# Kernel optimization log

Hardware: AMD Instinct MI355X
Metric: run time of the kernel (lower is better)

## Reference

```python
import jax, jax.numpy as jnp
import numpy as np

N_NODES = 100000
N_EDGES = 1000000
D_IN = 64
D_OUT = 64


def setup_inputs() -> dict:
    key = jax.random.key(0)
    k_x, k_e, k_w, k_b = jax.random.split(key, 4)
    x = jax.random.normal(k_x, (N_NODES, D_IN), dtype=jnp.float32)
    edge_index = jax.random.randint(k_e, (2, N_EDGES), 0, N_NODES, dtype=jnp.int64)
    # degrees of destination nodes (what the caller is expected to supply);
    # clamp to >=1 to avoid division by zero for isolated nodes
    deg = jax.ops.segment_sum(jnp.ones((N_EDGES,), jnp.float32), edge_index[1], num_segments=N_NODES)
    node_degrees = jnp.maximum(deg, 1.0)
    W = jax.random.normal(k_w, (D_OUT, D_IN), dtype=jnp.float32) * (1.0 / np.sqrt(D_IN))
    b = jax.random.normal(k_b, (D_OUT,), dtype=jnp.float32) * 0.01
    return {"x": x, "edge_index": edge_index, "node_degrees": node_degrees, "W": W, "b": b}


def reference(x, edge_index, node_degrees, W, b):
    # Original does argsort+cumsum+boundary segment-sum; mathematically this is
    # a scatter-add of gathered neighbor features into dst, i.e. a segment sum.
    src, dst = edge_index[0], edge_index[1]
    agg = jax.ops.segment_sum(x[src], dst, num_segments=x.shape[0])  # [N, D_IN]
    mean = agg / node_degrees[:, None]
    return mean @ W.T + b  # [N, D_OUT]
```

## Files before the change

### kernel.cpp

```cpp
#include <hip/hip_runtime.h>


#define D 64
#define BSHIFT 6
#define BNODES (1 << BSHIFT)
#define CAP 1024
#define GTHREADS 512
#define PERTHREAD (CAP / GTHREADS)
#define PXW_THREADS 512
#define MAXB 2048

__device__ inline int detect_stride_block(const unsigned* __restrict__ words,
                                          int E, int* sflag) {
    int t = threadIdx.x;
    if (t < 64) {
        unsigned v = (t < E) ? words[2 * t + 1] : 0u;
        int any = __any(v != 0u);
        if (t == 0) *sflag = any ? 1 : 2;
    }
    __syncthreads();
    return *sflag;
}

__device__ inline unsigned pack_bf16(float a, float b) {
    unsigned ua = __float_as_uint(a), ub = __float_as_uint(b);
    ua += 0x7fffu + ((ua >> 16) & 1u);
    ub += 0x7fffu + ((ub >> 16) & 1u);
    return (ua >> 16) | (ub & 0xffff0000u);
}

__global__ __launch_bounds__(PXW_THREADS, 4) void partition_xw_kernel(
        const unsigned* __restrict__ ewords, int* __restrict__ cursor,
        unsigned* __restrict__ pairs, uint2* __restrict__ spill,
        int* __restrict__ spillCnt,
        const float* __restrict__ x, const float* __restrict__ W,
        unsigned* __restrict__ y2, int E, int N, int nb, int pblocks) {
    __shared__ __align__(16) char smem[52240];
    int t = threadIdx.x;

    if ((int)blockIdx.x < pblocks) {
        int* lhist = (int*)smem;
        int* lbase = lhist + MAXB;
        int* sflag = lbase + MAXB;
        int s = detect_stride_block(ewords, E, sflag);
        int base = blockIdx.x * 8192;
        for (int i = t; i < nb; i += PXW_THREADS) lhist[i] = 0;
        __syncthreads();
        unsigned pv[16]; int bk[16];
        #pragma unroll
        for (int k = 0; k < 16; ++k) {
            int e = base + k * PXW_THREADS + t;
            bk[k] = -1;
            if (e < E) {
                unsigned src = ewords[(size_t)e * s];
                unsigned dst = ewords[((size_t)E + e) * s];
                bk[k] = (int)(dst >> BSHIFT);
                pv[k] = src | ((dst & (BNODES - 1)) << 17);
                atomicAdd(&lhist[bk[k]], 1);
            }
        }
        __syncthreads();
        for (int hb = t; hb < nb; hb += PXW_THREADS) {
            int cc = lhist[hb];
            if (cc) lbase[hb] = atomicAdd(&cursor[hb], cc);
            lhist[hb] = 0;
        }
        __syncthreads();
        #pragma unroll
        for (int k = 0; k < 16; ++k) {
            if (bk[k] >= 0) {
                int lpos = lbase[bk[k]] + atomicAdd(&lhist[bk[k]], 1);
                if (lpos < CAP) {
                    pairs[(size_t)bk[k] * CAP + lpos] = pv[k];
                } else {
                    int si = atomicAdd(spillCnt, 1);
                    unsigned dst = ((unsigned)bk[k] << BSHIFT) | (pv[k] >> 17);
                    spill[si] = make_uint2(pv[k] & 0x1FFFFu, dst);
                }
            }
        }
    } else {
        float* Wt = (float*)smem;
        float* xs = Wt + 64 * 68;
        for (int i = t; i < 64 * 64; i += PXW_THREADS) {
            int o = i >> 6, k = i & 63;
            Wt[k * 68 + o] = W[i];
        }
        int base = ((int)blockIdx.x - pblocks) * 128;
        int row = t >> 4, c4 = (t & 15) * 4;
        #pragma unroll
        for (int r = 0; r < 4; ++r) {
            int nl = row + r * 32;
            int n = base + nl;
            float4 v = {0.f, 0.f, 0.f, 0.f};
            if (n < N) v = *(const float4*)(x + (size_t)n * 64 + c4);
            *(float4*)&xs[nl * 68 + c4] = v;
        }
        __syncthreads();
        int o4 = (t & 15) * 4, nl4 = (t >> 4) * 4;
        float acc[4][4];
        #pragma unroll
        for (int i = 0; i < 4; ++i)
            #pragma unroll
            for (int j = 0; j < 4; ++j) acc[i][j] = 0.f;
        #pragma unroll 2
        for (int k0 = 0; k0 < 64; k0 += 4) {
            float a[4][4], wv[4][4];
            #pragma unroll
            for (int i = 0; i < 4; ++i)
                *(float4*)a[i] = *(const float4*)&xs[(nl4 + i) * 68 + k0];
            #pragma unroll
            for (int dk = 0; dk < 4; ++dk)
                *(float4*)wv[dk] = *(const float4*)&Wt[(k0 + dk) * 68 + o4];
            #pragma unroll
            for (int i = 0; i < 4; ++i)
                #pragma unroll
                for (int j = 0; j < 4; ++j)
                    acc[i][j] += a[i][0] * wv[0][j] + a[i][1] * wv[1][j]
                               + a[i][2] * wv[2][j] + a[i][3] * wv[3][j];
        }
        int n0 = base + nl4;
        #pragma unroll
        for (int i = 0; i < 4; ++i) {
            if (n0 + i < N) {
                uint2 p;
                p.x = pack_bf16(acc[i][0], acc[i][1]);
                p.y = pack_bf16(acc[i][2], acc[i][3]);
                *(uint2*)(y2 + (size_t)(n0 + i) * 32 + (o4 >> 1)) = p;
            }
        }
    }
}

__global__ __launch_bounds__(GTHREADS) void bucket_gather(
        const unsigned* __restrict__ y2, const unsigned* __restrict__ pairs,
        const int* __restrict__ cursor, const uint2* __restrict__ spill,
        const int* __restrict__ spillCnt,
        const float* __restrict__ deg, const float* __restrict__ b,
        float* __restrict__ out, int N) {
    __shared__ unsigned list[CAP];
    __shared__ int cnt[BNODES], st[BNODES], sc[BNODES];
    int t = threadIdx.x;
    int bkt = blockIdx.x, base = bkt << BSHIFT;
    int total = cursor[bkt];
    int cn = total < CAP ? total : CAP;
    int node = t >> 3, c = t & 7;
    float4 bv0 = ((const float4*)b)[c * 2];
    float4 bv1 = ((const float4*)b)[c * 2 + 1];

    if (t < BNODES) cnt[t] = 0;
    __syncthreads();
    unsigned pv[PERTHREAD];
    #pragma unroll
    for (int j = 0; j < PERTHREAD; ++j) {
        int i = t + j * GTHREADS;
        pv[j] = (i < cn) ? pairs[(size_t)bkt * CAP + i] : 0xFFFFFFFFu;
        if (pv[j] != 0xFFFFFFFFu) atomicAdd(&cnt[pv[j] >> 17], 1);
    }
    __syncthreads();
    if (t < 64) {
        int v = cnt[t];
        #pragma unroll
        for (int off = 1; off < 64; off <<= 1) {
            int u = __shfl_up(v, off);
            if (t >= off) v += u;
        }
        st[t] = v - cnt[t]; sc[t] = v - cnt[t];
    }
    __syncthreads();
    #pragma unroll
    for (int j = 0; j < PERTHREAD; ++j) {
        if (pv[j] != 0xFFFFFFFFu) {
            int pos = atomicAdd(&sc[pv[j] >> 17], 1);
            list[pos] = pv[j] & 0x1FFFFu;
        }
    }
    __syncthreads();

    int scnt = *spillCnt;

    int n = base + node;
    int s0 = st[node], e1 = s0 + cnt[node];
    float a0 = 0.f, a1 = 0.f, a2 = 0.f, a3 = 0.f;
    float a4 = 0.f, a5 = 0.f, a6 = 0.f, a7 = 0.f;
    float b0 = 0.f, b1 = 0.f, b2 = 0.f, b3 = 0.f;
    float b4 = 0.f, b5 = 0.f, b6 = 0.f, b7 = 0.f;
    int i = s0;
    for (; i + 1 < e1; i += 2) {
        unsigned s0v = list[i], s1v = list[i + 1];
        uint4 u0 = *(const uint4*)(y2 + (size_t)s0v * 32 + c * 4);
        uint4 u1 = *(const uint4*)(y2 + (size_t)s1v * 32 + c * 4);
        a0 += __uint_as_float(u0.x << 16);
        a1 += __uint_as_float(u0.x & 0xffff0000u);
        a2 += __uint_as_float(u0.y << 16);
        a3 += __uint_as_float(u0.y & 0xffff0000u);
        a4 += __uint_as_float(u0.z << 16);
        a5 += __uint_as_float(u0.z & 0xffff0000u);
        a6 += __uint_as_float(u0.w << 16);
        a7 += __uint_as_float(u0.w & 0xffff0000u);
        b0 += __uint_as_float(u1.x << 16);
        b1 += __uint_as_float(u1.x & 0xffff0000u);
        b2 += __uint_as_float(u1.y << 16);
        b3 += __uint_as_float(u1.y & 0xffff0000u);
        b4 += __uint_as_float(u1.z << 16);
        b5 += __uint_as_float(u1.z & 0xffff0000u);
        b6 += __uint_as_float(u1.w << 16);
        b7 += __uint_as_float(u1.w & 0xffff0000u);
    }
    if (i < e1) {
        unsigned sv = list[i];
        uint4 u = *(const uint4*)(y2 + (size_t)sv * 32 + c * 4);
        a0 += __uint_as_float(u.x << 16);
        a1 += __uint_as_float(u.x & 0xffff0000u);
        a2 += __uint_as_float(u.y << 16);
        a3 += __uint_as_float(u.y & 0xffff0000u);
        a4 += __uint_as_float(u.z << 16);
        a5 += __uint_as_float(u.z & 0xffff0000u);
        a6 += __uint_as_float(u.w << 16);
        a7 += __uint_as_float(u.w & 0xffff0000u);
    }
    a0 += b0; a1 += b1; a2 += b2; a3 += b3;
    a4 += b4; a5 += b5; a6 += b6; a7 += b7;
    for (int k = 0; k < scnt; ++k) {
        uint2 e = spill[k];
        if ((int)e.y == n) {
            uint4 u = *(const uint4*)(y2 + (size_t)e.x * 32 + c * 4);
            a0 += __uint_as_float(u.x << 16);
            a1 += __uint_as_float(u.x & 0xffff0000u);
            a2 += __uint_as_float(u.y << 16);
            a3 += __uint_as_float(u.y & 0xffff0000u);
            a4 += __uint_as_float(u.z << 16);
            a5 += __uint_as_float(u.z & 0xffff0000u);
            a6 += __uint_as_float(u.w << 16);
            a7 += __uint_as_float(u.w & 0xffff0000u);
        }
    }
    if (n < N) {
        float invd = 1.0f / deg[n];
        float4 o0 = {a0 * invd + bv0.x, a1 * invd + bv0.y,
                     a2 * invd + bv0.z, a3 * invd + bv0.w};
        float4 o1 = {a4 * invd + bv1.x, a5 * invd + bv1.y,
                     a6 * invd + bv1.z, a7 * invd + bv1.w};
        *(float4*)(out + (size_t)n * 64 + c * 8) = o0;
        *(float4*)(out + (size_t)n * 64 + c * 8 + 4) = o1;
    }
}

__global__ __launch_bounds__(256) void scatter_kernel(
        const float* __restrict__ x, const unsigned* __restrict__ ewords,
        float* __restrict__ agg, int E) {
    __shared__ int sflag;
    int s = detect_stride_block(ewords, E, &sflag);
    int gid = blockIdx.x * blockDim.x + threadIdx.x;
    int e = gid >> 4, q = gid & 15;
    if (e >= E) return;
    int src = (int)ewords[(size_t)e * s];
    int dst = (int)ewords[((size_t)E + e) * s];
    const float4 v = *(const float4*)(x + (size_t)src * D + q * 4);
    float* p = agg + (size_t)dst * D + q * 4;
    unsafeAtomicAdd(p + 0, v.x);
    unsafeAtomicAdd(p + 1, v.y);
    unsafeAtomicAdd(p + 2, v.z);
    unsafeAtomicAdd(p + 3, v.w);
}

__global__ __launch_bounds__(256) void gemm_kernel(
        float* __restrict__ inout, const float* __restrict__ deg,
        const float* __restrict__ W, const float* __restrict__ b, int nNodes) {
    __shared__ float Wt[64 * 65];
    __shared__ float rows[4 * 64];
    int t = threadIdx.x;
    for (int i = t; i < 64 * 64; i += 256) {
        int o = i >> 6, k = i & 63;
        Wt[k * 65 + o] = W[i];
    }
    int base = blockIdx.x * 4;
    int nl = t >> 6, o = t & 63;
    int n = base + nl;
    if (n < nNodes) {
        float invd = 1.0f / deg[n];
        rows[nl * 64 + o] = inout[(size_t)n * 64 + o] * invd;
    }
    __syncthreads();
    if (n >= nNodes) return;
    float acc = b[o];
    #pragma unroll
    for (int k = 0; k < 64; ++k)
        acc += rows[nl * 64 + k] * Wt[k * 65 + o];
    inout[(size_t)n * 64 + o] = acc;
}

extern "C" void kernel_launch(void* const* d_in, const int* in_sizes, int n_in,
                              void* d_out, int out_size, void* d_ws, size_t ws_size,
                              hipStream_t stream) {
    const float*    x      = (const float*)d_in[0];
    const unsigned* ewords = (const unsigned*)d_in[1];
    const float*    deg    = (const float*)d_in[2];
    const float*    W      = (const float*)d_in[3];
    const float*    b      = (const float*)d_in[4];
    float*          out    = (float*)d_out;

    const int E = in_sizes[1] / 2;
    const int N = in_sizes[2];
    const int nb = (N + BNODES - 1) >> BSHIFT;

    char* ws = (char*)d_ws;
    size_t curB  = (MAXB + 16) * 4;
    size_t pairB = ((size_t)nb * CAP * 4 + 63) & ~63ull;
    size_t spB   = ((size_t)E * 8 + 63) & ~63ull;
    size_t need  = curB + pairB + spB + (size_t)N * 32 * 4;

    if (ws_size >= need && N < (1 << 17) && nb <= MAXB) {
        int*      cursor   = (int*)ws;
        int*      spillCnt = cursor + MAXB;
        unsigned* pairs    = (unsigned*)(ws + curB);
        uint2*    spill    = (uint2*)(ws + curB + pairB);
        unsigned* y2       = (unsigned*)(ws + curB + pairB + spB);

        hipMemsetAsync(cursor, 0, curB, stream);

        int pblocks  = (E + 8191) / 8192;
        int xwblocks = (N + 127) / 128;
        partition_xw_kernel<<<pblocks + xwblocks, PXW_THREADS, 0, stream>>>(
            ewords, cursor, pairs, spill, spillCnt, x, W, y2, E, N, nb, pblocks);

        bucket_gather<<<nb, GTHREADS, 0, stream>>>(
            y2, pairs, cursor, spill, spillCnt, deg, b, out, N);
    } else {
        hipMemsetAsync(d_out, 0, (size_t)out_size * sizeof(float), stream);
        long long sthreads = (long long)E * 16;
        int sblocks = (int)((sthreads + 255) / 256);
        scatter_kernel<<<sblocks, 256, 0, stream>>>(x, ewords, out, E);
        gemm_kernel<<<(N + 3) / 4, 256, 0, stream>>>(out, deg, W, b, N);
    }
}
```

Baseline: 139.8 us.

## Balance bucket gather work by splitting edges evenly across thread groups

The bucket gather kernel no longer assigns one 8-thread group per destination node. It now splits the sorted edge list of each bucket evenly across the 64 groups. Each group accumulates runs of the same destination in registers and flushes partial sums into a shared-memory accumulator with LDS atomics, and a final pass reads the accumulator, adds spill edges and writes the output. This targets load imbalance from varying node degrees, at the cost of extra shared memory (about 17 KB), zero-initialisation, an extra barrier and atomic adds at segment boundaries.

Measured after the change: 183.0 us. +30.9%, slower.

```diff
diff --git a/kernel.cpp b/kernel.cpp
--- a/kernel.cpp
+++ b/kernel.cpp
@@ -140,22 +140,24 @@
         float* __restrict__ out, int N) {
     __shared__ unsigned list[CAP];
     __shared__ int cnt[BNODES], st[BNODES], sc[BNODES];
+    __shared__ float accum[BNODES * 68];
     int t = threadIdx.x;
     int bkt = blockIdx.x, base = bkt << BSHIFT;
     int total = cursor[bkt];
     int cn = total < CAP ? total : CAP;
-    int node = t >> 3, c = t & 7;
+    int c = t & 7, j = t >> 3;
     float4 bv0 = ((const float4*)b)[c * 2];
     float4 bv1 = ((const float4*)b)[c * 2 + 1];
 
     if (t < BNODES) cnt[t] = 0;
+    for (int i = t; i < BNODES * 68; i += GTHREADS) accum[i] = 0.f;
     __syncthreads();
     unsigned pv[PERTHREAD];
     #pragma unroll
-    for (int j = 0; j < PERTHREAD; ++j) {
-        int i = t + j * GTHREADS;
-        pv[j] = (i < cn) ? pairs[(size_t)bkt * CAP + i] : 0xFFFFFFFFu;
-        if (pv[j] != 0xFFFFFFFFu) atomicAdd(&cnt[pv[j] >> 17], 1);
+    for (int q = 0; q < PERTHREAD; ++q) {
+        int i = t + q * GTHREADS;
+        pv[q] = (i < cn) ? pairs[(size_t)bkt * CAP + i] : 0xFFFFFFFFu;
+        if (pv[q] != 0xFFFFFFFFu) atomicAdd(&cnt[pv[q] >> 17], 1);
     }
     __syncthreads();
     if (t < 64) {
@@ -169,73 +171,111 @@
     }
     __syncthreads();
     #pragma unroll
-    for (int j = 0; j < PERTHREAD; ++j) {
-        if (pv[j] != 0xFFFFFFFFu) {
-            int pos = atomicAdd(&sc[pv[j] >> 17], 1);
-            list[pos] = pv[j] & 0x1FFFFu;
-        }
+    for (int q = 0; q < PERTHREAD; ++q) {
+        if (pv[q] != 0xFFFFFFFFu) {
+            int pos = atomicAdd(&sc[pv[q] >> 17], 1);
+            list[pos] = pv[q];
+        }
+    }
+    __syncthreads();
+
+    int chunk = (cn + 63) >> 6;
+    int lo = j * chunk;
+    int hi = lo + chunk; if (hi > cn) hi = cn;
+    float s[8];
+    #pragma unroll
+    for (int k = 0; k < 8; ++k) s[k] = 0.f;
+    int cur = -1;
+    int i = lo;
+    for (; i + 1 < hi; i += 2) {
+        unsigned v0 = list[i], v1 = list[i + 1];
+        uint4 u0 = *(const uint4*)(y2 + (size_t)(v0 & 0x1FFFFu) * 32 + c * 4);
+        uint4 u1 = *(const uint4*)(y2 + (size_t)(v1 & 0x1FFFFu) * 32 + c * 4);
+        int nl0 = (int)(v0 >> 17), nl1 = (int)(v1 >> 17);
+        if (nl0 != cur) {
+            if (cur >= 0) {
+                float* ap = accum + cur * 68 + c * 8;
+                #pragma unroll
+                for (int k = 0; k < 8; ++k) atomicAdd(&ap[k], s[k]);
+            }
+            #pragma unroll
+            for (int k = 0; k < 8; ++k) s[k] = 0.f;
+            cur = nl0;
+        }
+        s[0] += __uint_as_float(u0.x << 16);
+        s[1] += __uint_as_float(u0.x & 0xffff0000u);
+        s[2] += __uint_as_float(u0.y << 16);
+        s[3] += __uint_as_float(u0.y & 0xffff0000u);
+        s[4] += __uint_as_float(u0.z << 16);
+        s[5] += __uint_as_float(u0.z & 0xffff0000u);
+        s[6] += __uint_as_float(u0.w << 16);
+        s[7] += __uint_as_float(u0.w & 0xffff0000u);
+        if (nl1 != cur) {
+            float* ap = accum + cur * 68 + c * 8;
+            #pragma unroll
+            for (int k = 0; k < 8; ++k) { atomicAdd(&ap[k], s[k]); s[k] = 0.f; }
+            cur = nl1;
+        }
+        s[0] += __uint_as_float(u1.x << 16);
+        s[1] += __uint_as_float(u1.x & 0xffff0000u);
+        s[2] += __uint_as_float(u1.y << 16);
+        s[3] += __uint_as_float(u1.y & 0xffff0000u);
+        s[4] += __uint_as_float(u1.z << 16);
+        s[5] += __uint_as_float(u1.z & 0xffff0000u);
+        s[6] += __uint_as_float(u1.w << 16);
+        s[7] += __uint_as_float(u1.w & 0xffff0000u);
+    }
+    if (i < hi) {
+        unsigned v0 = list[i];
+        uint4 u0 = *(const uint4*)(y2 + (size_t)(v0 & 0x1FFFFu) * 32 + c * 4);
+        int nl0 = (int)(v0 >> 17);
+        if (nl0 != cur) {
+            if (cur >= 0) {
+                float* ap = accum + cur * 68 + c * 8;
+                #pragma unroll
+                for (int k = 0; k < 8; ++k) atomicAdd(&ap[k], s[k]);
+            }
+            #pragma unroll
+            for (int k = 0; k < 8; ++k) s[k] = 0.f;
+            cur = nl0;
+        }
+        s[0] += __uint_as_float(u0.x << 16);
+        s[1] += __uint_as_float(u0.x & 0xffff0000u);
+        s[2] += __uint_as_float(u0.y << 16);
+        s[3] += __uint_as_float(u0.y & 0xffff0000u);
+        s[4] += __uint_as_float(u0.z << 16);
+        s[5] += __uint_as_float(u0.z & 0xffff0000u);
+        s[6] += __uint_as_float(u0.w << 16);
+        s[7] += __uint_as_float(u0.w & 0xffff0000u);
+    }
+    if (cur >= 0) {
+        float* ap = accum + cur * 68 + c * 8;
+        #pragma unroll
+        for (int k = 0; k < 8; ++k) atomicAdd(&ap[k], s[k]);
     }
     __syncthreads();
 
     int scnt = *spillCnt;
-
+    int node = j;
     int n = base + node;
-    int s0 = st[node], e1 = s0 + cnt[node];
-    float a0 = 0.f, a1 = 0.f, a2 = 0.f, a3 = 0.f;
-    float a4 = 0.f, a5 = 0.f, a6 = 0.f, a7 = 0.f;
-    float b0 = 0.f, b1 = 0.f, b2 = 0.f, b3 = 0.f;
-    float b4 = 0.f, b5 = 0.f, b6 = 0.f, b7 = 0.f;
-    int i = s0;
-    for (; i + 1 < e1; i += 2) {
-        unsigned s0v = list[i], s1v = list[i + 1];
-        uint4 u0 = *(const uint4*)(y2 + (size_t)s0v * 32 + c * 4);
-        uint4 u1 = *(const uint4*)(y2 + (size_t)s1v * 32 + c * 4);
-        a0 += __uint_as_float(u0.x << 16);
-        a1 += __uint_as_float(u0.x & 0xffff0000u);
-        a2 += __uint_as_float(u0.y << 16);
-        a3 += __uint_as_float(u0.y & 0xffff0000u);
-        a4 += __uint_as_float(u0.z << 16);
-        a5 += __uint_as_float(u0.z & 0xffff0000u);
-        a6 += __uint_as_float(u0.w << 16);
-        a7 += __uint_as_float(u0.w & 0xffff0000u);
-        b0 += __uint_as_float(u1.x << 16);
-        b1 += __uint_as_float(u1.x & 0xffff0000u);
-        b2 += __uint_as_float(u1.y << 16);
-        b3 += __uint_as_float(u1.y & 0xffff0000u);
-        b4 += __uint_as_float(u1.z << 16);
-        b5 += __uint_as_float(u1.z & 0xffff0000u);
-        b6 += __uint_as_float(u1.w << 16);
-        b7 += __uint_as_float(u1.w & 0xffff0000u);
-    }
-    if (i < e1) {
-        unsigned sv = list[i];
-        uint4 u = *(const uint4*)(y2 + (size_t)sv * 32 + c * 4);
-        a0 += __uint_as_float(u.x << 16);
-        a1 += __uint_as_float(u.x & 0xffff0000u);
-        a2 += __uint_as_float(u.y << 16);
-        a3 += __uint_as_float(u.y & 0xffff0000u);
-        a4 += __uint_as_float(u.z << 16);
-        a5 += __uint_as_float(u.z & 0xffff0000u);
-        a6 += __uint_as_float(u.w << 16);
-        a7 += __uint_as_float(u.w & 0xffff0000u);
-    }
-    a0 += b0; a1 += b1; a2 += b2; a3 += b3;
-    a4 += b4; a5 += b5; a6 += b6; a7 += b7;
-    for (int k = 0; k < scnt; ++k) {
-        uint2 e = spill[k];
-        if ((int)e.y == n) {
-            uint4 u = *(const uint4*)(y2 + (size_t)e.x * 32 + c * 4);
-            a0 += __uint_as_float(u.x << 16);
-            a1 += __uint_as_float(u.x & 0xffff0000u);
-            a2 += __uint_as_float(u.y << 16);
-            a3 += __uint_as_float(u.y & 0xffff0000u);
-            a4 += __uint_as_float(u.z << 16);
-            a5 += __uint_as_float(u.z & 0xffff0000u);
-            a6 += __uint_as_float(u.w << 16);
-            a7 += __uint_as_float(u.w & 0xffff0000u);
-        }
-    }
     if (n < N) {
+        const float* ap = accum + node * 68 + c * 8;
+        float a0 = ap[0], a1 = ap[1], a2 = ap[2], a3 = ap[3];
+        float a4 = ap[4], a5 = ap[5], a6 = ap[6], a7 = ap[7];
+        for (int k = 0; k < scnt; ++k) {
+            uint2 e = spill[k];
+            if ((int)e.y == n) {
+                uint4 u = *(const uint4*)(y2 + (size_t)e.x * 32 + c * 4);
+                a0 += __uint_as_float(u.x << 16);
+                a1 += __uint_as_float(u.x & 0xffff0000u);
+                a2 += __uint_as_float(u.y << 16);
+                a3 += __uint_as_float(u.y & 0xffff0000u);
+                a4 += __uint_as_float(u.z << 16);
+                a5 += __uint_as_float(u.z & 0xffff0000u);
+                a6 += __uint_as_float(u.w << 16);
+                a7 += __uint_as_float(u.w & 0xffff0000u);
+            }
+        }
         float invd = 1.0f / deg[n];
         float4 o0 = {a0 * invd + bv0.x, a1 * invd + bv0.y,
                      a2 * invd + bv0.z, a3 * invd + bv0.w};
```
